# Optimization experiments

Measured on AMD Instinct MI355X. Metric: run time of the kernel, lower is better.

Reference implementation:

```python
import jax, jax.numpy as jnp
import numpy as np

N, IN_DIM, OUT_DIM = 8192, 128, 64
NEG_INF = -9e15

def setup_inputs() -> dict:
    key = jax.random.key(0)
    k1, k2, k3, k4 = jax.random.split(key, 4)
    h = jax.random.normal(k1, (N, IN_DIM), dtype=jnp.float32)
    adj = jax.random.randint(k2, (N, N), 0, 2, dtype=jnp.int32)
    W = jax.random.normal(k3, (IN_DIM, OUT_DIM), dtype=jnp.float32) * (1.0 / np.sqrt(IN_DIM))
    a = jax.random.normal(k4, (2 * OUT_DIM,), dtype=jnp.float32)
    return {"h": h, "adj": adj, "W": W, "a": a}

def reference(h, adj, W, a):
    Wh = h @ W  # [N, F]
    F_ = Wh.shape[1]
    # additive decomposition of cat([Wh_i, Wh_j]) @ a == Wh_i@a1 + Wh_j@a2
    e_src = Wh @ a[:F_]   # [N]
    e_dst = Wh @ a[F_:]   # [N]
    e = jax.nn.leaky_relu(e_src[:, None] + e_dst[None, :], negative_slope=0.01)  # [N, N]
    attention = jnp.where(adj > 0, e, jnp.float32(NEG_INF))
    attention = jax.nn.softmax(attention, axis=1)
    h_prime = attention @ Wh  # [N, F]
    return jax.nn.elu(h_prime)
```

## Files before the change

kernel.cpp:

```cpp
#include <hip/hip_runtime.h>
#include <hip/hip_bf16.h>

typedef __attribute__((ext_vector_type(8))) short short8;
typedef __attribute__((ext_vector_type(4))) float f32x4;

#define NROW 8192
#define FDIM 64
#define INDIM 128
#define BK 64
#define BM 128
#define MBOUND 48.0f

static __device__ __forceinline__ short bfb(float x) {
  __hip_bfloat16 b = __float2bfloat16(x);
  return *reinterpret_cast<short*>(&b);
}
static __device__ __forceinline__ float lrelu(float x) { return fmaxf(x, 0.01f * x); }

__global__ __launch_bounds__(256) void k_wh(const float* __restrict__ h,
                                            const float* __restrict__ W,
                                            const float* __restrict__ a,
                                            __hip_bfloat16* __restrict__ WhT,
                                            float* __restrict__ s,
                                            float* __restrict__ d) {
  const int i = blockIdx.x * 4 + (threadIdx.x >> 6);
  const int f = threadIdx.x & 63;
  const float* hrow = h + (size_t)i * INDIM;
  float acc = 0.f;
#pragma unroll 8
  for (int k = 0; k < INDIM; ++k) acc = fmaf(hrow[k], W[k * FDIM + f], acc);
  WhT[(size_t)f * NROW + i] = __float2bfloat16(acc);
  float p1 = acc * a[f];
  float p2 = acc * a[FDIM + f];
#pragma unroll
  for (int m = 32; m; m >>= 1) {
    p1 += __shfl_xor(p1, m, 64);
    p2 += __shfl_xor(p2, m, 64);
  }
  if (f == 0) { s[i] = p1; d[i] = p2; }
}

__global__ __launch_bounds__(256, 4) void k_main(const int* __restrict__ adj,
                                                 const __hip_bfloat16* __restrict__ WhT,
                                                 const float* __restrict__ sArr,
                                                 const float* __restrict__ dArr,
                                                 float* __restrict__ accp,
                                                 float* __restrict__ Zp,
                                                 int splits) {
  const int t = threadIdx.x;
  const int w = t >> 6, l = t & 63;
  const int lr = l & 15;
  const int lk = l >> 4;
  const int panel = blockIdx.x / splits;
  const int split = blockIdx.x - panel * splits;
  const int row0 = panel * BM + w * 32;
  const int jspan = NROW / splits;
  const int j0 = split * jspan;
  const int nchunk = jspan / BK;

  const float s0 = sArr[row0 + lr];
  const float s1 = sArr[row0 + 16 + lr];
  const float m0 = lrelu(s0 + MBOUND);
  const float m1 = lrelu(s1 + MBOUND);

  f32x4 acc[2][4];
#pragma unroll
  for (int ri = 0; ri < 2; ++ri)
#pragma unroll
    for (int nf = 0; nf < 4; ++nf) acc[ri][nf] = (f32x4){0.f, 0.f, 0.f, 0.f};
  float z0 = 0.f, z1 = 0.f;

  const int* adj0 = adj + (size_t)row0 * NROW + j0 + l;
  const float* dp = dArr + j0 + lk * 8;
  const __hip_bfloat16* bbase = WhT + (size_t)lr * NROW + j0 + lk * 8;

  for (int c = 0; c < nchunk; ++c) {
    const int off = c * BK;

    unsigned long long M0 = 0ull, M1 = 0ull;
    {
      int av[16];
#pragma unroll
      for (int r = 0; r < 16; ++r) av[r] = adj0[(size_t)r * NROW + off];
#pragma unroll
      for (int r = 0; r < 16; ++r) {
        unsigned long long b = __ballot(av[r] > 0);
        M0 = (lr == r) ? b : M0;
      }
#pragma unroll
      for (int r = 0; r < 16; ++r) av[r] = adj0[(size_t)(16 + r) * NROW + off];
#pragma unroll
      for (int r = 0; r < 16; ++r) {
        unsigned long long b = __ballot(av[r] > 0);
        M1 = (lr == r) ? b : M1;
      }
    }

#pragma unroll
    for (int ks = 0; ks < 2; ++ks) {
      const int jo = off + ks * 32;
      const unsigned int y0 = (unsigned int)(M0 >> (ks * 32 + lk * 8)) & 0xffu;
      const unsigned int y1 = (unsigned int)(M1 >> (ks * 32 + lk * 8)) & 0xffu;

      short8 b0 = *(const short8*)(bbase + jo);
      short8 b1 = *(const short8*)(bbase + jo + 16 * NROW);
      short8 b2 = *(const short8*)(bbase + jo + 32 * NROW);
      short8 b3 = *(const short8*)(bbase + jo + 48 * NROW);

      float4 dv0 = *(const float4*)(dp + jo);
      float4 dv1 = *(const float4*)(dp + jo + 4);
      float dj[8] = {dv0.x, dv0.y, dv0.z, dv0.w, dv1.x, dv1.y, dv1.z, dv1.w};

      short8 pa0, pa1;
#pragma unroll
      for (int q = 0; q < 8; ++q) {
        const float dq = dj[q];
        float e0 = __expf(lrelu(s0 + dq) - m0);
        float e1 = __expf(lrelu(s1 + dq) - m1);
        float w0 = ((y0 >> q) & 1u) ? e0 : 0.f;
        float w1 = ((y1 >> q) & 1u) ? e1 : 0.f;
        z0 += w0;
        z1 += w1;
        pa0[q] = bfb(w0);
        pa1[q] = bfb(w1);
      }

      acc[0][0] = __builtin_amdgcn_mfma_f32_16x16x32_bf16(pa0, b0, acc[0][0], 0, 0, 0);
      acc[0][1] = __builtin_amdgcn_mfma_f32_16x16x32_bf16(pa0, b1, acc[0][1], 0, 0, 0);
      acc[0][2] = __builtin_amdgcn_mfma_f32_16x16x32_bf16(pa0, b2, acc[0][2], 0, 0, 0);
      acc[0][3] = __builtin_amdgcn_mfma_f32_16x16x32_bf16(pa0, b3, acc[0][3], 0, 0, 0);
      acc[1][0] = __builtin_amdgcn_mfma_f32_16x16x32_bf16(pa1, b0, acc[1][0], 0, 0, 0);
      acc[1][1] = __builtin_amdgcn_mfma_f32_16x16x32_bf16(pa1, b1, acc[1][1], 0, 0, 0);
      acc[1][2] = __builtin_amdgcn_mfma_f32_16x16x32_bf16(pa1, b2, acc[1][2], 0, 0, 0);
      acc[1][3] = __builtin_amdgcn_mfma_f32_16x16x32_bf16(pa1, b3, acc[1][3], 0, 0, 0);
    }
  }

  z0 += __shfl_xor(z0, 16, 64);
  z0 += __shfl_xor(z0, 32, 64);
  z1 += __shfl_xor(z1, 16, 64);
  z1 += __shfl_xor(z1, 32, 64);
  if (l < 16) {
    Zp[(size_t)blockIdx.x * BM + w * 32 + lr] = z0;
    Zp[(size_t)blockIdx.x * BM + w * 32 + 16 + lr] = z1;
  }

  float* ab = accp + (size_t)blockIdx.x * (BM * 64);
#pragma unroll
  for (int ri = 0; ri < 2; ++ri)
#pragma unroll
    for (int nf = 0; nf < 4; ++nf)
#pragma unroll
      for (int q = 0; q < 4; ++q)
        ab[(w * 32 + ri * 16 + lk * 4 + q) * 64 + nf * 16 + lr] = acc[ri][nf][q];
}

__global__ __launch_bounds__(256) void k_combine(const float* __restrict__ accp,
                                                 const float* __restrict__ Zp,
                                                 float* __restrict__ out,
                                                 int splits) {
  const int idx = blockIdx.x * 256 + threadIdx.x;
  const int r = idx >> 6, f = idx & 63;
  const int panel = r >> 7, rl = r & 127;
  float sum = 0.f, z = 0.f;
  for (int sp = 0; sp < splits; ++sp) {
    const int b = panel * splits + sp;
    sum += accp[(size_t)b * (BM * 64) + rl * 64 + f];
    z += Zp[(size_t)b * BM + rl];
  }
  const float v = sum / z;
  out[idx] = (v > 0.f) ? v : expm1f(v);
}

extern "C" void kernel_launch(void* const* d_in, const int* in_sizes, int n_in,
                              void* d_out, int out_size, void* d_ws, size_t ws_size,
                              hipStream_t stream) {
  const float* h = (const float*)d_in[0];
  const int* adj = (const int*)d_in[1];
  const float* W = (const float*)d_in[2];
  const float* a = (const float*)d_in[3];
  float* out = (float*)d_out;

  const int npanel = NROW / BM;
  int splits = 16;
  auto need = [&](int sp) -> size_t {
    return (size_t)1048576  + 65536  +
           (size_t)sp * npanel * BM * 4  +
           (size_t)sp * npanel * (BM * 64) * 4 ;
  };
  while (splits > 1 && need(splits) > ws_size) splits >>= 1;

  char* p = (char*)d_ws;
  __hip_bfloat16* WhT = (__hip_bfloat16*)p;
  float* s = (float*)(p + 1048576);
  float* d = (float*)(p + 1048576 + 32768);
  float* Zp = (float*)(p + 1048576 + 65536);
  float* accp = (float*)((char*)Zp + (size_t)splits * npanel * BM * 4);

  hipLaunchKernelGGL(k_wh, dim3(NROW / 4), dim3(256), 0, stream, h, W, a, WhT, s, d);
  hipLaunchKernelGGL(k_main, dim3(npanel * splits), dim3(256), 0, stream,
                     adj, WhT, s, d, accp, Zp, splits);
  hipLaunchKernelGGL(k_combine, dim3(out_size / 256), dim3(256), 0, stream,
                     accp, Zp, out, splits);
}
```

Measured before the change: 103.9 us.

## Pre-pack adjacency into bitmasks and use exp2 with folded log2e

A new pre-pass kernel reads the int32 adjacency matrix with 16-byte loads and packs it into 64-bit row bitmasks. The main attention kernel then loads one mask word per row per chunk, replacing the strided int32 loads and 32 ballots per chunk. The exponential becomes exp2f of an fmaf with the max and log2(e) pre-folded. The full adjacency read still happens, now in a separate kernel that cannot overlap with the main kernel's compute, and the workspace grows by an 8 MB bitmask.

```diff
diff --git a/kernel.cpp b/kernel.cpp
--- a/kernel.cpp
+++ b/kernel.cpp
@@ -9,13 +9,36 @@
 #define INDIM 128
 #define BK 64
 #define BM 128
+#define NW (NROW / 64)
 #define MBOUND 48.0f
+#define L2E 1.44269504f
 
 static __device__ __forceinline__ short bfb(float x) {
   __hip_bfloat16 b = __float2bfloat16(x);
   return *reinterpret_cast<short*>(&b);
 }
 static __device__ __forceinline__ float lrelu(float x) { return fmaxf(x, 0.01f * x); }
+
+__global__ __launch_bounds__(256) void k_pack(const int* __restrict__ adj,
+                                              unsigned long long* __restrict__ Ab) {
+  const int row = blockIdx.x * 4 + (threadIdx.x >> 6);
+  const int l = threadIdx.x & 63;
+  const int4* p = (const int4*)(adj + (size_t)row * NROW) + l;
+  const int lsh = 4 * (l & 7);
+  unsigned long long* abr = Ab + (size_t)row * NW;
+#pragma unroll 8
+  for (int it = 0; it < NROW / 256; ++it) {
+    int4 v = p[it * 64];
+    unsigned int nib = (unsigned int)((v.x & 1) | ((v.y & 1) << 1) | ((v.z & 1) << 2) | ((v.w & 1) << 3));
+    unsigned int val = nib << lsh;
+    val |= __shfl_xor(val, 1, 64);
+    val |= __shfl_xor(val, 2, 64);
+    val |= __shfl_xor(val, 4, 64);
+    unsigned int hi = __shfl_xor(val, 8, 64);
+    if ((l & 15) == 0)
+      abr[it * 4 + (l >> 4)] = (unsigned long long)val | ((unsigned long long)hi << 32);
+  }
+}
 
 __global__ __launch_bounds__(256) void k_wh(const float* __restrict__ h,
                                             const float* __restrict__ W,
@@ -40,7 +63,7 @@
   if (f == 0) { s[i] = p1; d[i] = p2; }
 }
 
-__global__ __launch_bounds__(256, 4) void k_main(const int* __restrict__ adj,
+__global__ __launch_bounds__(256, 4) void k_main(const unsigned long long* __restrict__ Ab,
                                                  const __hip_bfloat16* __restrict__ WhT,
                                                  const float* __restrict__ sArr,
                                                  const float* __restrict__ dArr,
@@ -60,8 +83,8 @@
 
   const float s0 = sArr[row0 + lr];
   const float s1 = sArr[row0 + 16 + lr];
-  const float m0 = lrelu(s0 + MBOUND);
-  const float m1 = lrelu(s1 + MBOUND);
+  const float sm0 = -lrelu(s0 + MBOUND) * L2E;
+  const float sm1 = -lrelu(s1 + MBOUND) * L2E;
 
   f32x4 acc[2][4];
 #pragma unroll
@@ -70,31 +93,15 @@
     for (int nf = 0; nf < 4; ++nf) acc[ri][nf] = (f32x4){0.f, 0.f, 0.f, 0.f};
   float z0 = 0.f, z1 = 0.f;
 
-  const int* adj0 = adj + (size_t)row0 * NROW + j0 + l;
+  const unsigned long long* ab0 = Ab + (size_t)(row0 + lr) * NW + j0 / 64;
+  const unsigned long long* ab1 = ab0 + (size_t)16 * NW;
   const float* dp = dArr + j0 + lk * 8;
   const __hip_bfloat16* bbase = WhT + (size_t)lr * NROW + j0 + lk * 8;
 
   for (int c = 0; c < nchunk; ++c) {
     const int off = c * BK;
-
-    unsigned long long M0 = 0ull, M1 = 0ull;
-    {
-      int av[16];
-#pragma unroll
-      for (int r = 0; r < 16; ++r) av[r] = adj0[(size_t)r * NROW + off];
-#pragma unroll
-      for (int r = 0; r < 16; ++r) {
-        unsigned long long b = __ballot(av[r] > 0);
-        M0 = (lr == r) ? b : M0;
-      }
-#pragma unroll
-      for (int r = 0; r < 16; ++r) av[r] = adj0[(size_t)(16 + r) * NROW + off];
-#pragma unroll
-      for (int r = 0; r < 16; ++r) {
-        unsigned long long b = __ballot(av[r] > 0);
-        M1 = (lr == r) ? b : M1;
-      }
-    }
+    const unsigned long long M0 = ab0[c];
+    const unsigned long long M1 = ab1[c];
 
 #pragma unroll
     for (int ks = 0; ks < 2; ++ks) {
@@ -115,8 +122,8 @@
 #pragma unroll
       for (int q = 0; q < 8; ++q) {
         const float dq = dj[q];
-        float e0 = __expf(lrelu(s0 + dq) - m0);
-        float e1 = __expf(lrelu(s1 + dq) - m1);
+        float e0 = exp2f(fmaf(lrelu(s0 + dq), L2E, sm0));
+        float e1 = exp2f(fmaf(lrelu(s1 + dq), L2E, sm1));
         float w0 = ((y0 >> q) & 1u) ? e0 : 0.f;
         float w1 = ((y1 >> q) & 1u) ? e1 : 0.f;
         z0 += w0;
@@ -186,7 +193,8 @@
   auto need = [&](int sp) -> size_t {
     return (size_t)1048576  + 65536  +
            (size_t)sp * npanel * BM * 4  +
-           (size_t)sp * npanel * (BM * 64) * 4 ;
+           (size_t)sp * npanel * (BM * 64) * 4  +
+           (size_t)NROW * NW * 8 ;
   };
   while (splits > 1 && need(splits) > ws_size) splits >>= 1;
 
@@ -196,10 +204,12 @@
   float* d = (float*)(p + 1048576 + 32768);
   float* Zp = (float*)(p + 1048576 + 65536);
   float* accp = (float*)((char*)Zp + (size_t)splits * npanel * BM * 4);
-
+  unsigned long long* Ab = (unsigned long long*)((char*)accp + (size_t)splits * npanel * (BM * 64) * 4);
+
+  hipLaunchKernelGGL(k_pack, dim3(NROW / 4), dim3(256), 0, stream, adj, Ab);
   hipLaunchKernelGGL(k_wh, dim3(NROW / 4), dim3(256), 0, stream, h, W, a, WhT, s, d);
   hipLaunchKernelGGL(k_main, dim3(npanel * splits), dim3(256), 0, stream,
-                     adj, WhT, s, d, accp, Zp, splits);
+                     Ab, WhT, s, d, accp, Zp, splits);
   hipLaunchKernelGGL(k_combine, dim3(out_size / 256), dim3(256), 0, stream,
                      accp, Zp, out, splits);
 }
```

Measured after the change: 153.4 us. +47.6%, slower.
